# Kernel tuning notes

Hardware: AMD Instinct MI355X
Metric: run time of the kernel (lower is better)

The kernel has to match this reference:

```python
import jax, jax.numpy as jnp
import numpy as np

NUM_HEADS = 4
NUM_GROUPS = 8
EPS = 1e-5


def group_norm(x, gamma, beta):
    # x: [b, c, h, w], GroupNorm with NUM_GROUPS groups, eps=1e-5
    b, c, h, w = x.shape
    xg = x.reshape(b, NUM_GROUPS, (c // NUM_GROUPS) * h * w)
    mean = jnp.mean(xg, axis=-1, keepdims=True)
    var = jnp.var(xg, axis=-1, keepdims=True)
    xn = ((xg - mean) * jax.lax.rsqrt(var + EPS)).reshape(b, c, h, w)
    return xn * gamma[None, :, None, None] + beta[None, :, None, None]


def setup_inputs() -> dict:
    key = jax.random.key(0)
    ks = jax.random.split(key, 4)
    b, c, h, w = 4, 256, 64, 64
    x = jax.random.normal(ks[0], (b, c, h, w), dtype=jnp.float32)
    gamma = jnp.ones((c,), dtype=jnp.float32)
    beta = jnp.zeros((c,), dtype=jnp.float32)
    w_qkv = jax.random.normal(ks[1], (3 * c, c), dtype=jnp.float32) * (c ** -0.5)
    b_qkv = jnp.zeros((3 * c,), dtype=jnp.float32)
    w_proj = jax.random.normal(ks[2], (c, c), dtype=jnp.float32) * (c ** -0.5)
    b_proj = jnp.zeros((c,), dtype=jnp.float32)
    return {"x": x, "gamma": gamma, "beta": beta, "w_qkv": w_qkv,
            "b_qkv": b_qkv, "w_proj": w_proj, "b_proj": b_proj}


def reference(x, gamma, beta, w_qkv, b_qkv, w_proj, b_proj):
    b, c, h, w = x.shape
    heads = NUM_HEADS
    dim = c // heads
    n = h * w
    residual = x
    xn = group_norm(x, gamma, beta)
    # 1x1 conv == per-pixel linear: [b,c,h,w] x [3c,c] -> [b,3c,h,w]
    qkv = jnp.einsum('bchw,oc->bohw', xn, w_qkv) + b_qkv[None, :, None, None]
    # channel layout: (three, heads, dim)
    qkv = qkv.reshape(b, 3, heads, dim, n)            # [b,3,H,D,N]
    qkv = jnp.transpose(qkv, (1, 0, 2, 4, 3))         # [3,b,H,N,D]
    q, k, v = qkv[0], qkv[1], qkv[2]
    scale = dim ** -0.5
    scores = jnp.einsum('bhid,bhjd->bhij', q * scale, k)  # [b,H,N,N]
    attn = jax.nn.softmax(scores, axis=-1)
    out = jnp.einsum('bhij,bhjd->bhid', attn, v)          # [b,H,N,D]
    out = jnp.transpose(out, (0, 1, 3, 2)).reshape(b, c, h, w)
    out = jnp.einsum('bchw,oc->bohw', out, w_proj) + b_proj[None, :, None, None]
    return out + residual
```

## Files before the change

kernel.cpp:

```cpp
#include <hip/hip_runtime.h>
#include <stdint.h>

typedef unsigned short ushort_t;
typedef __attribute__((ext_vector_type(8))) short bf16x8;
typedef __attribute__((ext_vector_type(4))) float f32x4;
typedef __attribute__((ext_vector_type(16))) float f32x16;
typedef __attribute__((ext_vector_type(4))) unsigned int u32x4;

__device__ __forceinline__ ushort_t f2bf(float f) {
  union { float f; unsigned u; } v; v.f = f;
  unsigned r = v.u + 0x7fffu + ((v.u >> 16) & 1u);
  return (ushort_t)(r >> 16);
}
__device__ __forceinline__ unsigned bfbits(float f) {
  union { float f; unsigned u; } v; v.f = f; return v.u;
}
__device__ __forceinline__ unsigned pack_trunc(float lo, float hi) {
#if __has_builtin(__builtin_amdgcn_perm)
  return __builtin_amdgcn_perm(bfbits(hi), bfbits(lo), 0x07060302u);
#else
  return (bfbits(lo) >> 16) | (bfbits(hi) & 0xffff0000u);
#endif
}
__device__ __forceinline__ unsigned pack_rn(float lo, float hi) {
  return (unsigned)f2bf(lo) | ((unsigned)f2bf(hi) << 16);
}
__device__ __forceinline__ void swap32(unsigned &a, unsigned &b) {
#if __has_builtin(__builtin_amdgcn_permlane32_swap)
  auto r = __builtin_amdgcn_permlane32_swap(a, b, false, false);
  a = r[0]; b = r[1];
#else
  asm volatile("v_permlane32_swap_b32 %0, %1" : "+v"(a), "+v"(b));
#endif
}

#define SCALE_Q 0.18033688011112042f
#define EXP_BIAS 23.083109273961734f

__global__ __launch_bounds__(256)
void gn_stats1(const float* __restrict__ x, float2* __restrict__ partial) {
  int blk = blockIdx.x, tid = threadIdx.x;
  const float* base = x + (size_t)blk * 16384;
  float s = 0.f, ss = 0.f;
  for (int i = tid * 4; i < 16384; i += 1024) {
    float4 v = *(const float4*)(base + i);
    s  += v.x + v.y + v.z + v.w;
    ss += v.x*v.x + v.y*v.y + v.z*v.z + v.w*v.w;
  }
  __shared__ float rs[256], rss[256];
  rs[tid] = s; rss[tid] = ss;
  __syncthreads();
  for (int off = 128; off > 0; off >>= 1) {
    if (tid < off) { rs[tid] += rs[tid+off]; rss[tid] += rss[tid+off]; }
    __syncthreads();
  }
  if (tid == 0) partial[blk] = make_float2(rs[0], rss[0]);
}

__global__ __launch_bounds__(64)
void gn_stats2(const float2* __restrict__ partial, float* __restrict__ stats) {
  int g = threadIdx.x;
  if (g < 32) {
    float s = 0.f, ss = 0.f;
    #pragma unroll
    for (int k = 0; k < 8; k++) { float2 p = partial[g*8 + k]; s += p.x; ss += p.y; }
    float mean = s * (1.f/131072.f);
    float var  = ss * (1.f/131072.f) - mean*mean;
    stats[g*2]   = mean;
    stats[g*2+1] = rsqrtf(var + 1e-5f);
  }
}

__global__ __launch_bounds__(256)
void gn_apply_t(const float* __restrict__ x, const float* __restrict__ stats,
                const float* __restrict__ gamma, const float* __restrict__ beta,
                ushort_t* __restrict__ xn_t, int b0) {
  int blk = blockIdx.x;
  int tid = threadIdx.x;
  int ct = blk & 7;
  int nt = (blk >> 3) & 15;
  int bl = blk >> 7;
  int b  = b0 + bl;
  int c0 = ct * 32;
  float mean = stats[(b*8 + ct)*2];
  float rstd = stats[(b*8 + ct)*2 + 1];
  __shared__ ushort_t Ls[32][264];
  for (int idx = tid; idx < 32*64; idx += 256) {
    int cc = idx >> 6, seg = idx & 63;
    float ga = gamma[c0+cc], be = beta[c0+cc];
    float a = rstd * ga;
    float bb = be - mean * a;
    float4 v = *(const float4*)(x + ((size_t)(b*256 + c0 + cc))*4096 + nt*256 + seg*4);
    ushort4 t4 = make_ushort4(f2bf(v.x*a+bb), f2bf(v.y*a+bb), f2bf(v.z*a+bb), f2bf(v.w*a+bb));
    *(ushort4*)&Ls[cc][seg*4] = t4;
  }
  __syncthreads();
  for (int idx = tid; idx < 256*4; idx += 256) {
    int n = idx >> 2, seg = idx & 3;
    union { ushort_t u[8]; uint4 v; } pk;
    #pragma unroll
    for (int e = 0; e < 8; e++) pk.u[e] = Ls[seg*8 + e][n];
    *(uint4*)(xn_t + ((size_t)(bl*4096 + nt*256 + n))*256 + c0 + seg*8) = pk.v;
  }
}

__global__ __launch_bounds__(256)
void wconv2(const float* __restrict__ wq, const float* __restrict__ wp,
            ushort_t* __restrict__ oq, ushort_t* __restrict__ op) {
  int blk = blockIdx.x;
  const float* w; ushort_t* o; int i;
  if (blk < 192) { w = wq; o = oq; i = blk*256 + threadIdx.x; }
  else           { w = wp; o = op; i = (blk-192)*256 + threadIdx.x; }
  float4 v = *(const float4*)(w + (size_t)i*4);
  *(ushort4*)(o + (size_t)i*4) = make_ushort4(f2bf(v.x), f2bf(v.y), f2bf(v.z), f2bf(v.w));
}

__global__ __launch_bounds__(256)
void gemm_qkv(const ushort_t* __restrict__ A, const ushort_t* __restrict__ Bt,
              const float* __restrict__ bias, ushort_t* __restrict__ q,
              ushort_t* __restrict__ kbuf, ushort_t* __restrict__ vt, int b0) {
  int blk = blockIdx.x;
  int nt = blk % 12, mt = blk / 12;
  int m0 = mt*128, n0 = nt*64;
  int tid = threadIdx.x;
  int wave = tid >> 6, lane = tid & 63, quad = lane >> 4, l16 = lane & 15;
  __shared__ ushort_t As[128][40];
  __shared__ ushort_t Bs[64][40];
  __shared__ ushort_t Lt[64][136];
  f32x4 acc[2][4];
  #pragma unroll
  for (int i = 0; i < 2; i++)
    #pragma unroll
    for (int j = 0; j < 4; j++) acc[i][j] = (f32x4){0.f,0.f,0.f,0.f};

  for (int k0 = 0; k0 < 256; k0 += 32) {
    #pragma unroll
    for (int i = tid; i < 512; i += 256) {
      int row = i >> 2, seg = i & 3;
      *(uint4*)&As[row][seg*8] = *(const uint4*)(A + (size_t)(m0+row)*256 + k0 + seg*8);
    }
    {
      int row = tid >> 2, seg = tid & 3;
      *(uint4*)&Bs[row][seg*8] = *(const uint4*)(Bt + (size_t)(n0+row)*256 + k0 + seg*8);
    }
    __syncthreads();
    bf16x8 af[2], bfr[4];
    #pragma unroll
    for (int t = 0; t < 2; t++) af[t]  = *(const bf16x8*)&As[wave*32 + t*16 + l16][quad*8];
    #pragma unroll
    for (int t = 0; t < 4; t++) bfr[t] = *(const bf16x8*)&Bs[t*16 + l16][quad*8];
    #pragma unroll
    for (int ti = 0; ti < 2; ti++)
      #pragma unroll
      for (int jn = 0; jn < 4; jn++)
        acc[ti][jn] = __builtin_amdgcn_mfma_f32_16x16x32_bf16(af[ti], bfr[jn], acc[ti][jn], 0, 0, 0);
    __syncthreads();
  }

  int region = nt >> 2;
  if (region == 0) {
    #pragma unroll
    for (int jn = 0; jn < 4; jn++) {
      int n = n0 + jn*16 + l16;
      float bv = bias[n];
      #pragma unroll
      for (int ti = 0; ti < 2; ti++) {
        int mrow = m0 + wave*32 + ti*16 + quad*4;
        #pragma unroll
        for (int r = 0; r < 4; r++)
          q[(size_t)(b0*4096 + mrow + r)*256 + n] = f2bf((acc[ti][jn][r] + bv) * SCALE_Q);
      }
    }
  } else if (region == 1) {
    #pragma unroll
    for (int jn = 0; jn < 4; jn++) {
      int n = n0 + jn*16 + l16;
      float bv = bias[n];
      #pragma unroll
      for (int ti = 0; ti < 2; ti++) {
        int mrow = m0 + wave*32 + ti*16 + quad*4;
        #pragma unroll
        for (int r = 0; r < 4; r++)
          kbuf[(size_t)(b0*4096 + mrow + r)*256 + (n - 256)] = f2bf(acc[ti][jn][r] + bv);
      }
    }
  } else {
    int hh = nt - 8;
    int b_loc = m0 >> 12;
    #pragma unroll
    for (int jn = 0; jn < 4; jn++) {
      int n = n0 + jn*16 + l16;
      float bv = bias[n];
      int drow = jn*16 + l16;
      #pragma unroll
      for (int ti = 0; ti < 2; ti++) {
        int tcol = wave*32 + ti*16 + quad*4;
        uint2 w;
        w.x = pack_rn(acc[ti][jn][0] + bv, acc[ti][jn][1] + bv);
        w.y = pack_rn(acc[ti][jn][2] + bv, acc[ti][jn][3] + bv);
        *(uint2*)&Lt[drow][tcol] = w;
      }
    }
    __syncthreads();
    size_t vb_ = ((size_t)((b0 + b_loc)*4 + hh)*64)*4096 + (size_t)(m0 & 4095);
    for (int idx = tid; idx < 1024; idx += 256) {
      int dd = idx >> 4, toff = (idx & 15)*8;
      *(uint4*)(vt + vb_ + (size_t)dd*4096 + toff) = *(const uint4*)&Lt[dd][toff];
    }
  }
}

__global__ __launch_bounds__(256, 2)
void attn(ushort_t* __restrict__ q, const ushort_t* __restrict__ k,
          const ushort_t* __restrict__ vt) {
  int blk = blockIdx.x;
  int it = blk & 31;
  int h  = (blk >> 5) & 3;
  int b  = blk >> 7;
  int i0 = it * 128;
  int tid = threadIdx.x;
  int wave = tid >> 6, lane = tid & 63;
  int q32 = lane & 31, hi = lane >> 5;

  __shared__ ushort_t Ks[2][128][72];
  __shared__ ushort_t Vs[2][64][144];

  const ushort_t* kbase = k + (size_t)(b*4096)*256 + h*64;
  const ushort_t* vbase = vt + (size_t)(b*4 + h)*64*4096;
  ushort_t* qrow = q + (size_t)(b*4096 + i0 + wave*32 + q32)*256 + h*64;

  bf16x8 qb0 = *(const bf16x8*)(qrow      + hi*8);
  bf16x8 qb1 = *(const bf16x8*)(qrow + 16 + hi*8);
  bf16x8 qb2 = *(const bf16x8*)(qrow + 32 + hi*8);
  bf16x8 qb3 = *(const bf16x8*)(qrow + 48 + hi*8);

  bf16x8 ones;
  #pragma unroll
  for (int e = 0; e < 8; e++) ones[e] = (short)0x3F80;

  f32x16 bias_init;
  #pragma unroll
  for (int r = 0; r < 16; r++) bias_init[r] = -EXP_BIAS;

  f32x16 o_acc0, o_acc1, l_acc;
  #pragma unroll
  for (int r = 0; r < 16; r++) { o_acc0[r] = 0.f; o_acc1[r] = 0.f; l_acc[r] = 0.f; }

  int sr = tid >> 3, sc = (tid & 7) * 8;
  int vr = tid >> 4, vc = (tid & 15) * 8;
  uint4 rk0, rk1, rk2, rk3, rv0, rv1, rv2, rv3;
  #define LOADK(JT) { int j0n = (JT)*128; \
    rk0 = *(const uint4*)(kbase + (size_t)(j0n + sr      )*256 + sc); \
    rk1 = *(const uint4*)(kbase + (size_t)(j0n + sr + 32 )*256 + sc); \
    rk2 = *(const uint4*)(kbase + (size_t)(j0n + sr + 64 )*256 + sc); \
    rk3 = *(const uint4*)(kbase + (size_t)(j0n + sr + 96 )*256 + sc); }
  #define WRITEK(BI) { \
    *(uint4*)&Ks[BI][sr      ][sc] = rk0; \
    *(uint4*)&Ks[BI][sr + 32 ][sc] = rk1; \
    *(uint4*)&Ks[BI][sr + 64 ][sc] = rk2; \
    *(uint4*)&Ks[BI][sr + 96 ][sc] = rk3; }
  #define LOADV(JT) { int j0n = (JT)*128; \
    rv0 = *(const uint4*)(vbase + (size_t)(vr     )*4096 + j0n + vc); \
    rv1 = *(const uint4*)(vbase + (size_t)(vr + 16)*4096 + j0n + vc); \
    rv2 = *(const uint4*)(vbase + (size_t)(vr + 32)*4096 + j0n + vc); \
    rv3 = *(const uint4*)(vbase + (size_t)(vr + 48)*4096 + j0n + vc); }
  #define WRITEV(BI) { \
    *(uint4*)&Vs[BI][vr     ][vc] = rv0; \
    *(uint4*)&Vs[BI][vr + 16][vc] = rv1; \
    *(uint4*)&Vs[BI][vr + 32][vc] = rv2; \
    *(uint4*)&Vs[BI][vr + 48][vc] = rv3; }

  #define COMPUTE_SUB32(BI, JB) { \
    bf16x8 kb0 = *(const bf16x8*)&Ks[BI][(JB) + q32][hi*8]; \
    bf16x8 kb1 = *(const bf16x8*)&Ks[BI][(JB) + q32][16 + hi*8]; \
    bf16x8 kb2 = *(const bf16x8*)&Ks[BI][(JB) + q32][32 + hi*8]; \
    bf16x8 kb3 = *(const bf16x8*)&Ks[BI][(JB) + q32][48 + hi*8]; \
    f32x16 s_ = __builtin_amdgcn_mfma_f32_32x32x16_bf16(kb0, qb0, bias_init, 0, 0, 0); \
    s_ = __builtin_amdgcn_mfma_f32_32x32x16_bf16(kb1, qb1, s_, 0, 0, 0); \
    s_ = __builtin_amdgcn_mfma_f32_32x32x16_bf16(kb2, qb2, s_, 0, 0, 0); \
    s_ = __builtin_amdgcn_mfma_f32_32x32x16_bf16(kb3, qb3, s_, 0, 0, 0); \
    _Pragma("unroll") \
    for (int r = 0; r < 16; r++) s_[r] = __builtin_exp2f(s_[r]); \
    unsigned pkA = pack_trunc(s_[0],  s_[1]),  pkB = pack_trunc(s_[2],  s_[3]); \
    unsigned pkC = pack_trunc(s_[4],  s_[5]),  pkD = pack_trunc(s_[6],  s_[7]); \
    unsigned pkE = pack_trunc(s_[8],  s_[9]),  pkF = pack_trunc(s_[10], s_[11]); \
    unsigned pkG = pack_trunc(s_[12], s_[13]), pkH = pack_trunc(s_[14], s_[15]); \
    swap32(pkA, pkC); swap32(pkB, pkD);    \
    swap32(pkE, pkG); swap32(pkF, pkH);    \
    u32x4 w0_ = {pkA, pkB, pkC, pkD}; \
    u32x4 w1_ = {pkE, pkF, pkG, pkH}; \
    bf16x8 pb0 = __builtin_bit_cast(bf16x8, w0_); \
    bf16x8 pb1 = __builtin_bit_cast(bf16x8, w1_); \
    bf16x8 vb00 = *(const bf16x8*)&Vs[BI][q32     ][(JB) + hi*8]; \
    bf16x8 vb01 = *(const bf16x8*)&Vs[BI][q32     ][(JB) + 16 + hi*8]; \
    bf16x8 vb10 = *(const bf16x8*)&Vs[BI][32 + q32][(JB) + hi*8]; \
    bf16x8 vb11 = *(const bf16x8*)&Vs[BI][32 + q32][(JB) + 16 + hi*8]; \
    o_acc0 = __builtin_amdgcn_mfma_f32_32x32x16_bf16(vb00, pb0, o_acc0, 0, 0, 0); \
    o_acc0 = __builtin_amdgcn_mfma_f32_32x32x16_bf16(vb01, pb1, o_acc0, 0, 0, 0); \
    o_acc1 = __builtin_amdgcn_mfma_f32_32x32x16_bf16(vb10, pb0, o_acc1, 0, 0, 0); \
    o_acc1 = __builtin_amdgcn_mfma_f32_32x32x16_bf16(vb11, pb1, o_acc1, 0, 0, 0); \
    l_acc  = __builtin_amdgcn_mfma_f32_32x32x16_bf16(ones, pb0, l_acc, 0, 0, 0); \
    l_acc  = __builtin_amdgcn_mfma_f32_32x32x16_bf16(ones, pb1, l_acc, 0, 0, 0); \
  }

  LOADK(0); LOADV(0); WRITEK(0); WRITEV(0);
  __syncthreads();

  for (int jt = 0; jt < 32; jt++) {
    int cur = jt & 1;
    if (jt < 31) LOADK(jt + 1);
    COMPUTE_SUB32(cur, 0)
    COMPUTE_SUB32(cur, 32)
    if (jt < 31) { WRITEK(cur ^ 1); LOADV(jt + 1); }
    COMPUTE_SUB32(cur, 64)
    COMPUTE_SUB32(cur, 96)
    if (jt < 31) WRITEV(cur ^ 1);
    __syncthreads();
  }
  #undef LOADK
  #undef LOADV
  #undef WRITEK
  #undef WRITEV
  #undef COMPUTE_SUB32

  float inv = 1.f / l_acc[0];

  #pragma unroll
  for (int g = 0; g < 4; g++) {
    ushort4 u;
    u.x = f2bf(o_acc0[g*4+0]*inv); u.y = f2bf(o_acc0[g*4+1]*inv);
    u.z = f2bf(o_acc0[g*4+2]*inv); u.w = f2bf(o_acc0[g*4+3]*inv);
    *(ushort4*)(qrow + g*8 + hi*4) = u;
  }
  #pragma unroll
  for (int g = 0; g < 4; g++) {
    ushort4 u;
    u.x = f2bf(o_acc1[g*4+0]*inv); u.y = f2bf(o_acc1[g*4+1]*inv);
    u.z = f2bf(o_acc1[g*4+2]*inv); u.w = f2bf(o_acc1[g*4+3]*inv);
    *(ushort4*)(qrow + 32 + g*8 + hi*4) = u;
  }
}

__global__ __launch_bounds__(256)
void gemm_proj(const ushort_t* __restrict__ A,
               const ushort_t* __restrict__ Bt,
               const float* __restrict__ bias, const float* __restrict__ resid,
               float* __restrict__ out, int col_base) {
  int blk = blockIdx.x;
  int mt = blk & 1, nt = blk >> 1;
  int m0 = mt*128, n0 = nt*64;
  int tid = threadIdx.x;
  int wave = tid >> 6, lane = tid & 63, quad = lane >> 4, l16 = lane & 15;
  __shared__ ushort_t As[128][40];
  __shared__ ushort_t Bs[64][40];
  f32x4 acc[2][4];
  #pragma unroll
  for (int i = 0; i < 2; i++)
    #pragma unroll
    for (int j = 0; j < 4; j++) acc[i][j] = (f32x4){0.f,0.f,0.f,0.f};

  for (int k0 = 0; k0 < 256; k0 += 32) {
    #pragma unroll
    for (int i = tid; i < 512; i += 256) {
      int row = i >> 2, seg = i & 3;
      *(uint4*)&As[row][seg*8] = *(const uint4*)(A + (size_t)(m0+row)*256 + k0 + seg*8);
    }
    {
      int row = tid >> 2, seg = tid & 3;
      *(uint4*)&Bs[row][seg*8] = *(const uint4*)(Bt + (size_t)(n0+row)*256 + k0 + seg*8);
    }
    __syncthreads();
    bf16x8 af[2], bfr[4];
    #pragma unroll
    for (int t = 0; t < 2; t++) af[t]  = *(const bf16x8*)&As[wave*32 + t*16 + l16][quad*8];
    #pragma unroll
    for (int t = 0; t < 4; t++) bfr[t] = *(const bf16x8*)&Bs[t*16 + l16][quad*8];
    #pragma unroll
    for (int ti = 0; ti < 2; ti++)
      #pragma unroll
      for (int jn = 0; jn < 4; jn++)
        acc[ti][jn] = __builtin_amdgcn_mfma_f32_16x16x32_bf16(af[ti], bfr[jn], acc[ti][jn], 0, 0, 0);
    __syncthreads();
  }
  #pragma unroll
  for (int jn = 0; jn < 4; jn++) {
    int col = col_base + n0 + jn*16 + l16;
    int bb = col >> 12;
    int np = col & 4095;
    #pragma unroll
    for (int ti = 0; ti < 2; ti++) {
      int o = m0 + wave*32 + ti*16 + quad*4;
      #pragma unroll
      for (int r = 0; r < 4; r++) {
        int oo = o + r;
        size_t addr = ((size_t)(bb*256 + oo))*4096 + np;
        out[addr] = acc[ti][jn][r] + bias[oo] + resid[addr];
      }
    }
  }
}

extern "C" void kernel_launch(void* const* d_in, const int* in_sizes, int n_in,
                              void* d_out, int out_size, void* d_ws, size_t ws_size,
                              hipStream_t stream) {
  const float* x      = (const float*)d_in[0];
  const float* gamma  = (const float*)d_in[1];
  const float* beta   = (const float*)d_in[2];
  const float* w_qkv  = (const float*)d_in[3];
  const float* b_qkv  = (const float*)d_in[4];
  const float* w_proj = (const float*)d_in[5];
  const float* b_proj = (const float*)d_in[6];
  float* out = (float*)d_out;

  char* ws = (char*)d_ws;
  float*  stats    = (float*)ws;
  float2* partial  = (float2*)(ws + 1024);
  ushort_t* wqkv_bf  = (ushort_t*)(ws + 4096);
  ushort_t* wproj_bf = (ushort_t*)(ws + 397312);
  char* big = ws + 528384;

  gn_stats1<<<dim3(256), dim3(256), 0, stream>>>(x, partial);
  gn_stats2<<<dim3(1), dim3(64), 0, stream>>>(partial, stats);
  wconv2<<<dim3(256), dim3(256), 0, stream>>>(w_qkv, w_proj, wqkv_bf, wproj_bf);

  if (ws_size >= (size_t)528384 + 3*(size_t)8388608 + (size_t)4194304) {
    ushort_t* q    = (ushort_t*)big;
    ushort_t* kbuf = (ushort_t*)(big + (size_t)8388608);
    ushort_t* vt   = (ushort_t*)(big + (size_t)16777216);
    ushort_t* xn   = (ushort_t*)(big + (size_t)25165824);
    for (int c = 0; c < 2; c++) {
      int b0 = c * 2;
      gn_apply_t<<<dim3(256), dim3(256), 0, stream>>>(x, stats, gamma, beta, xn, b0);
      gemm_qkv<<<dim3(768), dim3(256), 0, stream>>>(xn, wqkv_bf, b_qkv, q, kbuf, vt, b0);
    }
    attn<<<dim3(512), dim3(256), 0, stream>>>(q, kbuf, vt);
    gemm_proj<<<dim3(512), dim3(256), 0, stream>>>(wproj_bf, q, b_proj, x, out, 0);
  } else {
    ushort_t* q_c  = (ushort_t*)big;
    ushort_t* k_c  = (ushort_t*)(big + (size_t)2097152);
    ushort_t* vt_c = (ushort_t*)(big + (size_t)4194304);
    ushort_t* xn_c = (ushort_t*)(big + (size_t)6291456);
    for (int b0 = 0; b0 < 4; b0++) {
      gn_apply_t<<<dim3(128), dim3(256), 0, stream>>>(x, stats, gamma, beta, xn_c, b0);
      gemm_qkv<<<dim3(384), dim3(256), 0, stream>>>(xn_c, wqkv_bf, b_qkv, q_c, k_c, vt_c, 0);
      attn<<<dim3(128), dim3(256), 0, stream>>>(q_c, k_c, vt_c);
      gemm_proj<<<dim3(128), dim3(256), 0, stream>>>(wproj_bf, q_c, b_proj, x, out, b0*4096);
    }
  }
}
```

Before: 247.5 us.

## Shrink attention KV tile to 64 keys, raise occupancy, add MFMA priority

Halves the K/V shared-memory tile from 128 to 64 keys per iteration, which cuts LDS use enough to request 4 blocks per CU instead of 2. The loop runs 64 iterations with two 32-key sub-blocks each, and the global loads and LDS writes are re-split across threads. It also raises wave priority around the MFMA/exp section with s_setprio. The aim is more concurrent waves to hide latency, at the cost of twice as many barriers and a tighter register budget that may cause spills.

```diff
diff --git a/kernel.cpp b/kernel.cpp
--- a/kernel.cpp
+++ b/kernel.cpp
@@ -210,7 +210,7 @@
   }
 }
 
-__global__ __launch_bounds__(256, 2)
+__global__ __launch_bounds__(256, 4)
 void attn(ushort_t* __restrict__ q, const ushort_t* __restrict__ k,
           const ushort_t* __restrict__ vt) {
   int blk = blockIdx.x;
@@ -222,8 +222,8 @@
   int wave = tid >> 6, lane = tid & 63;
   int q32 = lane & 31, hi = lane >> 5;
 
-  __shared__ ushort_t Ks[2][128][72];
-  __shared__ ushort_t Vs[2][64][144];
+  __shared__ ushort_t Ks[2][64][72];
+  __shared__ ushort_t Vs[2][64][72];
 
   const ushort_t* kbase = k + (size_t)(b*4096)*256 + h*64;
   const ushort_t* vbase = vt + (size_t)(b*4 + h)*64*4096;
@@ -246,35 +246,27 @@
   #pragma unroll
   for (int r = 0; r < 16; r++) { o_acc0[r] = 0.f; o_acc1[r] = 0.f; l_acc[r] = 0.f; }
 
-  int sr = tid >> 3, sc = (tid & 7) * 8;
-  int vr = tid >> 4, vc = (tid & 15) * 8;
-  uint4 rk0, rk1, rk2, rk3, rv0, rv1, rv2, rv3;
-  #define LOADK(JT) { int j0n = (JT)*128; \
-    rk0 = *(const uint4*)(kbase + (size_t)(j0n + sr      )*256 + sc); \
-    rk1 = *(const uint4*)(kbase + (size_t)(j0n + sr + 32 )*256 + sc); \
-    rk2 = *(const uint4*)(kbase + (size_t)(j0n + sr + 64 )*256 + sc); \
-    rk3 = *(const uint4*)(kbase + (size_t)(j0n + sr + 96 )*256 + sc); }
+  int sr = tid >> 2, sc = (tid & 3) * 16;
+  uint4 rk0, rk1, rv0, rv1;
+  #define LOADK(JT) { int j0n = (JT)*64; \
+    rk0 = *(const uint4*)(kbase + (size_t)(j0n + sr)*256 + sc); \
+    rk1 = *(const uint4*)(kbase + (size_t)(j0n + sr)*256 + sc + 8); }
   #define WRITEK(BI) { \
-    *(uint4*)&Ks[BI][sr      ][sc] = rk0; \
-    *(uint4*)&Ks[BI][sr + 32 ][sc] = rk1; \
-    *(uint4*)&Ks[BI][sr + 64 ][sc] = rk2; \
-    *(uint4*)&Ks[BI][sr + 96 ][sc] = rk3; }
-  #define LOADV(JT) { int j0n = (JT)*128; \
-    rv0 = *(const uint4*)(vbase + (size_t)(vr     )*4096 + j0n + vc); \
-    rv1 = *(const uint4*)(vbase + (size_t)(vr + 16)*4096 + j0n + vc); \
-    rv2 = *(const uint4*)(vbase + (size_t)(vr + 32)*4096 + j0n + vc); \
-    rv3 = *(const uint4*)(vbase + (size_t)(vr + 48)*4096 + j0n + vc); }
+    *(uint4*)&Ks[BI][sr][sc]     = rk0; \
+    *(uint4*)&Ks[BI][sr][sc + 8] = rk1; }
+  #define LOADV(JT) { int j0n = (JT)*64; \
+    rv0 = *(const uint4*)(vbase + (size_t)sr*4096 + j0n + sc); \
+    rv1 = *(const uint4*)(vbase + (size_t)sr*4096 + j0n + sc + 8); }
   #define WRITEV(BI) { \
-    *(uint4*)&Vs[BI][vr     ][vc] = rv0; \
-    *(uint4*)&Vs[BI][vr + 16][vc] = rv1; \
-    *(uint4*)&Vs[BI][vr + 32][vc] = rv2; \
-    *(uint4*)&Vs[BI][vr + 48][vc] = rv3; }
+    *(uint4*)&Vs[BI][sr][sc]     = rv0; \
+    *(uint4*)&Vs[BI][sr][sc + 8] = rv1; }
 
   #define COMPUTE_SUB32(BI, JB) { \
     bf16x8 kb0 = *(const bf16x8*)&Ks[BI][(JB) + q32][hi*8]; \
     bf16x8 kb1 = *(const bf16x8*)&Ks[BI][(JB) + q32][16 + hi*8]; \
     bf16x8 kb2 = *(const bf16x8*)&Ks[BI][(JB) + q32][32 + hi*8]; \
     bf16x8 kb3 = *(const bf16x8*)&Ks[BI][(JB) + q32][48 + hi*8]; \
+    __builtin_amdgcn_s_setprio(1); \
     f32x16 s_ = __builtin_amdgcn_mfma_f32_32x32x16_bf16(kb0, qb0, bias_init, 0, 0, 0); \
     s_ = __builtin_amdgcn_mfma_f32_32x32x16_bf16(kb1, qb1, s_, 0, 0, 0); \
     s_ = __builtin_amdgcn_mfma_f32_32x32x16_bf16(kb2, qb2, s_, 0, 0, 0); \
@@ -301,20 +293,19 @@
     o_acc1 = __builtin_amdgcn_mfma_f32_32x32x16_bf16(vb11, pb1, o_acc1, 0, 0, 0); \
     l_acc  = __builtin_amdgcn_mfma_f32_32x32x16_bf16(ones, pb0, l_acc, 0, 0, 0); \
     l_acc  = __builtin_amdgcn_mfma_f32_32x32x16_bf16(ones, pb1, l_acc, 0, 0, 0); \
+    __builtin_amdgcn_s_setprio(0); \
   }
 
   LOADK(0); LOADV(0); WRITEK(0); WRITEV(0);
   __syncthreads();
 
-  for (int jt = 0; jt < 32; jt++) {
+  for (int jt = 0; jt < 64; jt++) {
     int cur = jt & 1;
-    if (jt < 31) LOADK(jt + 1);
+    if (jt < 63) LOADK(jt + 1);
     COMPUTE_SUB32(cur, 0)
+    if (jt < 63) { WRITEK(cur ^ 1); LOADV(jt + 1); }
     COMPUTE_SUB32(cur, 32)
-    if (jt < 31) { WRITEK(cur ^ 1); LOADV(jt + 1); }
-    COMPUTE_SUB32(cur, 64)
-    COMPUTE_SUB32(cur, 96)
-    if (jt < 31) WRITEV(cur ^ 1);
+    if (jt < 63) WRITEV(cur ^ 1);
     __syncthreads();
   }
   #undef LOADK
```

New measurement: 413.9 us. +67.2%, slower.
